# Kernel optimization log

Measured on AMD Instinct MI355X. Metric: run time of the kernel, lower is better.

## Reference

```python
import jax, jax.numpy as jnp
import numpy as np

D_MODEL = 1024
D_STATE = 64
BATCH = 4
SEQ_L = 4096
LN_EPS = 1e-5


def setup_inputs() -> dict:
    key = jax.random.key(0)
    ks = jax.random.split(key, 8)
    u = jax.random.normal(ks[0], (BATCH, SEQ_L, D_MODEL), jnp.float32)
    # Parameters mirroring StateSpaceLayer._initialize_parameters
    A_log = jax.random.uniform(ks[1], (D_STATE,), jnp.float32, -2.0, -0.1)
    xav = float(np.sqrt(6.0 / (D_STATE + D_MODEL)))
    B = jax.random.uniform(ks[2], (D_STATE, D_MODEL), jnp.float32, -xav, xav) * 0.1
    C = jax.random.uniform(ks[3], (D_MODEL, D_STATE), jnp.float32, -xav, xav) * 0.1
    D = jnp.zeros((D_MODEL,), jnp.float32)
    delta = jax.random.uniform(ks[4], (D_MODEL,), jnp.float32, 0.001, 0.1)
    gamma = jnp.ones((D_MODEL,), jnp.float32)
    beta = jnp.zeros((D_MODEL,), jnp.float32)
    freq_align = jax.random.normal(ks[5], (D_MODEL,), jnp.float32)
    reward = jax.random.normal(ks[6], (D_MODEL,), jnp.float32)
    return dict(u=u, A_log=A_log, B=B, C=C, D=D, delta=delta,
                gamma=gamma, beta=beta, freq_align=freq_align, reward=reward)


def reference(u, A_log, B, C, D, delta, gamma, beta, freq_align, reward):
    b, L, d = u.shape
    A = -jnp.exp(A_log)                                   # [N]
    # --- convolution kernel: K[k] = C @ (A_bar[0])^k, A_bar[0] = exp(delta[0]*A) ---
    k_idx = jnp.arange(L, dtype=u.dtype)                  # [L]
    powers = jnp.exp(k_idx[:, None] * (delta[0] * A)[None, :])  # [L, N]
    K = jnp.einsum('ln,dn->ld', powers, C)                # [L, D]
    # --- FFT-based causal (circular, zero-padded) convolution ---
    fft_size = 1 << int(np.ceil(np.log2(2 * L)))
    u_fft = jnp.fft.fft(u, n=fft_size, axis=1)            # [B, F, D] complex
    K_fft = jnp.fft.fft(K, n=fft_size, axis=0)            # [F, D] complex
    y = jnp.fft.ifft(u_fft * K_fft[None], axis=1).real[:, :L, :]
    # --- D skip connection ---
    y = y + u * D
    # --- FFT-based learning signals: scale spectrum, add real 'reward' to every bin ---
    y_fft = jnp.fft.fft(y, axis=1)
    y = jnp.fft.ifft(y_fft * freq_align + reward, axis=1).real
    # --- LayerNorm (eval-mode dropout = identity) ---
    mean = y.mean(-1, keepdims=True)
    var = y.var(-1, keepdims=True)
    y = (y - mean) / jnp.sqrt(var + LN_EPS) * gamma + beta
    # --- final state update with mean timescale ---
    delta_mean = delta.mean()
    A_bar_s = jnp.exp(delta_mean * A)                     # [N]
    A_safe = A + 1e-8 * jnp.sign(A)
    B_bar = ((A_bar_s - 1.0) / A_safe)[:, None] * B       # [N, D]
    state = jnp.zeros((b, A.shape[0]), u.dtype)
    final_state = A_bar_s * state + jnp.einsum('nd,bd->bn', B_bar, u[:, -1, :])
    return (y, final_state)
```

## Files before the change

### kernel.cpp

```cpp
#include <hip/hip_runtime.h>
#include <math.h>

#define BATCH  4
#define SEQL   4096
#define DMODEL 1024
#define NSTATE 64
#define LN_EPS 1e-5f
#define NCH    16
#define TCH    256
#define TB     16
#define TSUB   8

typedef unsigned short u16;
typedef unsigned int   u32;
typedef float f32x2 __attribute__((ext_vector_type(2)));

__device__ __forceinline__ f32x2 fma2(f32x2 a, f32x2 b, f32x2 c) {
#if __has_builtin(__builtin_elementwise_fma)
    return __builtin_elementwise_fma(a, b, c);
#else
    f32x2 d; d.x = fmaf(a.x, b.x, c.x); d.y = fmaf(a.y, b.y, c.y); return d;
#endif
}

__device__ __forceinline__ u16 f2bf(float x) {
    u32 b = __float_as_uint(x);
    b += 0x7FFF + ((b >> 16) & 1);
    return (u16)(b >> 16);
}
__device__ __forceinline__ float bf2f(u16 h) {
    return __uint_as_float(((u32)h) << 16);
}
__device__ __forceinline__ f32x2 unpack2bf(u32 p) {
    f32x2 v; v.x = bf2f((u16)p); v.y = bf2f((u16)(p >> 16)); return v;
}

template <bool ZBF16>
__global__ __launch_bounds__(256) void k_scan(const float* __restrict__ u,
                                              const float* __restrict__ A_log,
                                              const float* __restrict__ C,
                                              const float* __restrict__ Dvec,
                                              const float* __restrict__ delta,
                                              const float* __restrict__ fal,
                                              const float* __restrict__ rw,
                                              const float* __restrict__ Bm,
                                              u16* __restrict__ f,
                                              void* __restrict__ zout,
                                              float* __restrict__ st,
                                              int nb) {
    if (blockIdx.x >= nb) {
        const int sb = blockIdx.x - nb;
        const int n = sb & 63;
        const int b = sb >> 6;
        const int tid = threadIdx.x;
        const float* ul = u + ((size_t)b * SEQL + (SEQL - 1)) * DMODEL;
        const float* Bn = Bm + (size_t)n * DMODEL;
        float dot = 0.f, dsum = 0.f;
        for (int dd = tid; dd < DMODEL; dd += 256) {
            dot = fmaf(Bn[dd], ul[dd], dot);
            dsum += delta[dd];
        }
#pragma unroll
        for (int off = 32; off > 0; off >>= 1) {
            dot  += __shfl_down(dot,  off, 64);
            dsum += __shfl_down(dsum, off, 64);
        }
        __shared__ float red[8];
        const int wave = tid >> 6, lane = tid & 63;
        if (lane == 0) { red[wave] = dot; red[4 + wave] = dsum; }
        __syncthreads();
        if (tid == 0) {
            dot  = red[0] + red[1] + red[2] + red[3];
            dsum = red[4] + red[5] + red[6] + red[7];
            const float dmean = dsum * (1.f / DMODEL);
            const float A = -expf(A_log[n]);
            const float Abar = expf(dmean * A);
            const float Asafe = A + (A >= 0.f ? 1e-8f : -1e-8f);
            st[sb] = ((Abar - 1.f) / Asafe) * dot;
        }
        return;
    }
    __shared__ float r_lds[NSTATE];
    __shared__ float part[2][4][TB][64];
    const int tid = threadIdx.x;
    const int w = tid >> 6, l = tid & 63;
    const int b   = blockIdx.x / (16 * NCH);
    const int rem = blockIdx.x % (16 * NCH);
    const int dt  = rem / NCH;
    const int j   = rem % NCH;
    const int n0  = w << 4;
    const int d   = (dt << 6) | l;

    if (tid < NSTATE) r_lds[tid] = expf(delta[0] * -expf(A_log[tid]));
    __syncthreads();

    const float fad = fal[d];
    f32x2 r2[8], c2[8], s2[8];
#pragma unroll
    for (int p = 0; p < 8; ++p) {
        r2[p] = *(const f32x2*)&r_lds[n0 + 2 * p];
        s2[p] = (f32x2)(0.f, 0.f);
    }
#pragma unroll
    for (int p = 0; p < 8; ++p) {
        c2[p].x = fad * C[(size_t)d * NSTATE + n0 + 2*p];
        c2[p].y = fad * C[(size_t)d * NSTATE + n0 + 2*p + 1];
    }

    const float Ddf = Dvec[d] * fad;
    const float rwd = rw[d];
    const float* ub = u + ((size_t)b * SEQL + (size_t)j * TCH) * DMODEL + d;
    const size_t zoff = ((size_t)b * SEQL + (size_t)j * TCH) * DMODEL + d;
    u16*   zb16 = (u16*)zout + zoff;
    float* zb32 = (float*)zout + zoff;

    for (int tb = 0; tb < TCH / TB; ++tb) {
        const int pb = tb & 1;
        float ur[TB];
        f32x2 zr2[TB];
#pragma unroll
        for (int t = 0; t < TB; ++t) {
            ur[t] = ub[(size_t)(tb * TB + t) * DMODEL];
            zr2[t] = (f32x2)(0.f, 0.f);
        }
#pragma unroll
        for (int q = 0; q < 4; ++q) {
            f32x2 sa = s2[2*q], sb2 = s2[2*q+1];
            const f32x2 ra = r2[2*q], rb = r2[2*q+1];
            const f32x2 ca = c2[2*q], cb = c2[2*q+1];
#pragma unroll
            for (int t = 0; t < TB; ++t) {
                f32x2 u2; u2.x = ur[t]; u2.y = ur[t];
                sa  = fma2(ra, sa,  u2);
                sb2 = fma2(rb, sb2, u2);
                zr2[t] = fma2(ca, sa,  zr2[t]);
                zr2[t] = fma2(cb, sb2, zr2[t]);
            }
            s2[2*q] = sa; s2[2*q+1] = sb2;
        }
#pragma unroll
        for (int t = 0; t < TB; ++t) {
            float v = zr2[t].x + zr2[t].y;
            if (w == 0) v = fmaf(Ddf, ur[t], v);
            part[pb][w][t][l] = v;
        }
        __syncthreads();
#pragma unroll
        for (int k = 0; k < 4; ++k) {
            const int t = (w << 2) | k;
            float v = (part[pb][0][t][l] + part[pb][1][t][l]) +
                      (part[pb][2][t][l] + part[pb][3][t][l]);
            if (j == 0 && tb == 0 && t == 0) v += rwd;
            if (ZBF16) zb16[(size_t)(tb * TB + t) * DMODEL] = f2bf(v);
            else       zb32[(size_t)(tb * TB + t) * DMODEL] = v;
        }
    }
    u16* fb = f + (((size_t)b * NCH + j) * NSTATE + n0) * DMODEL + d;
#pragma unroll
    for (int p = 0; p < 8; ++p) {
        fb[(size_t)(2*p)     * DMODEL] = f2bf(s2[p].x);
        fb[(size_t)(2*p + 1) * DMODEL] = f2bf(s2[p].y);
    }
}

__global__ __launch_bounds__(256) void k_pass2w(const float* __restrict__ A_log,
                                                const float* __restrict__ delta,
                                                const float* __restrict__ C,
                                                const float* __restrict__ fal,
                                                u16* __restrict__ f) {
    const int tid = blockIdx.x * 256 + threadIdx.x;
    const int d = tid & (DMODEL - 1);
    const int n = (tid >> 10) & (NSTATE - 1);
    const int b = tid >> 16;
    const float A  = -expf(A_log[n]);
    const float rT = expf((float)TCH * delta[0] * A);
    const float fc = fal[d] * C[(size_t)d * NSTATE + n];
    float I = 0.f;
    u16* p = f + ((size_t)b * NCH * NSTATE + n) * DMODEL + d;
    const size_t stride = (size_t)NSTATE * DMODEL;
    for (int j = 0; j < NCH; ++j) {
        float tmp = bf2f(p[(size_t)j * stride]);
        p[(size_t)j * stride] = f2bf(fc * I);
        I = fmaf(rT, I, tmp);
    }
}

template <bool ZBF16>
__global__ __launch_bounds__(256) void k_corr_ln(const void* __restrict__ zin,
                                                 const u16* __restrict__ W,
                                                 const float* __restrict__ A_log,
                                                 const float* __restrict__ delta,
                                                 const float* __restrict__ gamma,
                                                 const float* __restrict__ beta,
                                                 float* __restrict__ y) {
    const int lb  = (blockIdx.x & 7) * 256 + (blockIdx.x >> 3);
    const int b   = lb >> 9;
    const int row = lb & 511;
    const int tbase = row * TSUB;
    const int j     = tbase >> 8;
    const int tloc0 = tbase & (TCH - 1);

    __shared__ float r_lds[NSTATE];
    __shared__ float pst_lds[NSTATE];
    __shared__ float red[4 * TSUB * 2];

    const int tid = threadIdx.x;
    if (tid < NSTATE) {
        const float A = -expf(A_log[tid]);
        const float d0v = delta[0];
        r_lds[tid]   = expf(d0v * A);
        pst_lds[tid] = expf((float)(tloc0 + 1) * d0v * A);
    }
    __syncthreads();

    const int d0 = tid << 2;
    f32x2 acc01[TSUB], acc23[TSUB];
#pragma unroll
    for (int t = 0; t < TSUB; ++t) {
        acc01[t] = (f32x2)(0.f, 0.f);
        acc23[t] = (f32x2)(0.f, 0.f);
    }

    if (j > 0) {
        const u16* Wb = W + (((size_t)b * NCH + j) * NSTATE) * DMODEL + d0;
#pragma unroll 2
        for (int n = 0; n < NSTATE; ++n) {
            const uint2 wv = *(const uint2*)(Wb + (size_t)n * DMODEL);
            const f32x2 w01 = unpack2bf(wv.x);
            const f32x2 w23 = unpack2bf(wv.y);
            float p = pst_lds[n];
            const float r = r_lds[n];
#pragma unroll
            for (int t = 0; t < TSUB; ++t) {
                f32x2 pp; pp.x = p; pp.y = p;
                acc01[t] = fma2(pp, w01, acc01[t]);
                acc23[t] = fma2(pp, w23, acc23[t]);
                p *= r;
            }
        }
    }

    const size_t rowoff = ((size_t)b * SEQL + tbase) * DMODEL + d0;
    float sums[TSUB], sqs[TSUB];
#pragma unroll
    for (int t = 0; t < TSUB; ++t) {
        float z0, z1, z2, z3;
        if (ZBF16) {
            const uint2 zv = *(const uint2*)((const u16*)zin + rowoff + (size_t)t * DMODEL);
            const f32x2 a = unpack2bf(zv.x), bb2 = unpack2bf(zv.y);
            z0 = a.x; z1 = a.y; z2 = bb2.x; z3 = bb2.y;
        } else {
            const float4 zv = *(const float4*)((const float*)zin + rowoff + (size_t)t * DMODEL);
            z0 = zv.x; z1 = zv.y; z2 = zv.z; z3 = zv.w;
        }
        z0 += acc01[t].x; z1 += acc01[t].y; z2 += acc23[t].x; z3 += acc23[t].y;
        acc01[t].x = z0; acc01[t].y = z1; acc23[t].x = z2; acc23[t].y = z3;
        sums[t] = (z0 + z1) + (z2 + z3);
        sqs[t]  = (z0*z0 + z1*z1) + (z2*z2 + z3*z3);
    }
    const int wave = tid >> 6, lane = tid & 63;
#pragma unroll
    for (int t = 0; t < TSUB; ++t) {
        float s = sums[t], q = sqs[t];
#pragma unroll
        for (int off = 32; off > 0; off >>= 1) {
            s += __shfl_down(s, off, 64);
            q += __shfl_down(q, off, 64);
        }
        if (lane == 0) {
            red[(wave * TSUB + t) * 2]     = s;
            red[(wave * TSUB + t) * 2 + 1] = q;
        }
    }
    __syncthreads();
    const float4 g  = *(const float4*)&gamma[d0];
    const float4 bb = *(const float4*)&beta[d0];
#pragma unroll
    for (int t = 0; t < TSUB; ++t) {
        float s = red[t * 2]     + red[(TSUB + t) * 2] +
                  red[(2 * TSUB + t) * 2] + red[(3 * TSUB + t) * 2];
        float q = red[t * 2 + 1] + red[(TSUB + t) * 2 + 1] +
                  red[(2 * TSUB + t) * 2 + 1] + red[(3 * TSUB + t) * 2 + 1];
        const float mean = s * (1.f / DMODEL);
        const float var  = q * (1.f / DMODEL) - mean * mean;
        const float inv  = 1.f / sqrtf(var + LN_EPS);
        float4 o;
        o.x = (acc01[t].x - mean) * inv * g.x + bb.x;
        o.y = (acc01[t].y - mean) * inv * g.y + bb.y;
        o.z = (acc23[t].x - mean) * inv * g.z + bb.z;
        o.w = (acc23[t].y - mean) * inv * g.w + bb.w;
        *(float4*)&y[rowoff + (size_t)t * DMODEL] = o;
    }
}

extern "C" void kernel_launch(void* const* d_in, const int* in_sizes, int n_in,
                              void* d_out, int out_size, void* d_ws, size_t ws_size,
                              hipStream_t stream) {
    const float* u     = (const float*)d_in[0];
    const float* A_log = (const float*)d_in[1];
    const float* B     = (const float*)d_in[2];
    const float* C     = (const float*)d_in[3];
    const float* Dv    = (const float*)d_in[4];
    const float* delta = (const float*)d_in[5];
    const float* gamma = (const float*)d_in[6];
    const float* beta  = (const float*)d_in[7];
    const float* fal   = (const float*)d_in[8];
    const float* rw    = (const float*)d_in[9];

    float* y  = (float*)d_out;
    float* st = y + (size_t)BATCH * SEQL * DMODEL;
    u16* f    = (u16*)d_ws;

    const int nb = BATCH * 16 * NCH;

    const size_t f_bytes = (size_t)BATCH * NCH * NSTATE * DMODEL * sizeof(u16);
    const size_t z_bytes = (size_t)BATCH * SEQL * DMODEL * sizeof(u16);
    const bool zbf16 = (f_bytes + z_bytes) <= ws_size;
    void* zbuf = zbf16 ? (void*)((char*)d_ws + f_bytes) : (void*)y;

    if (zbf16) {
        hipLaunchKernelGGL((k_scan<true>), dim3(nb + BATCH * NSTATE), dim3(256), 0, stream,
                           u, A_log, C, Dv, delta, fal, rw, B, f, zbuf, st, nb);
    } else {
        hipLaunchKernelGGL((k_scan<false>), dim3(nb + BATCH * NSTATE), dim3(256), 0, stream,
                           u, A_log, C, Dv, delta, fal, rw, B, f, zbuf, st, nb);
    }
    hipLaunchKernelGGL(k_pass2w, dim3(BATCH * NSTATE * DMODEL / 256), dim3(256), 0, stream,
                       A_log, delta, C, fal, f);
    if (zbf16) {
        hipLaunchKernelGGL((k_corr_ln<true>), dim3(BATCH * (SEQL / TSUB)), dim3(256), 0, stream,
                           zbuf, f, A_log, delta, gamma, beta, y);
    } else {
        hipLaunchKernelGGL((k_corr_ln<false>), dim3(BATCH * (SEQL / TSUB)), dim3(256), 0, stream,
                           zbuf, f, A_log, delta, gamma, beta, y);
    }
}
```

Before: 115.2 us.

## Compute chunk correction with bf16 MFMA and transpose carry-state layout

```diff
diff --git a/kernel.cpp b/kernel.cpp
--- a/kernel.cpp
+++ b/kernel.cpp
@@ -9,11 +9,14 @@
 #define NCH    16
 #define TCH    256
 #define TB     16
-#define TSUB   8
+#define TSUB   16
+#define PPAD   80
 
 typedef unsigned short u16;
 typedef unsigned int   u32;
 typedef float f32x2 __attribute__((ext_vector_type(2)));
+typedef float f32x4 __attribute__((ext_vector_type(4)));
+typedef short bf16x8 __attribute__((ext_vector_type(8)));
 
 __device__ __forceinline__ f32x2 fma2(f32x2 a, f32x2 b, f32x2 c) {
 #if __has_builtin(__builtin_elementwise_fma)
@@ -31,8 +34,8 @@
 __device__ __forceinline__ float bf2f(u16 h) {
     return __uint_as_float(((u32)h) << 16);
 }
-__device__ __forceinline__ f32x2 unpack2bf(u32 p) {
-    f32x2 v; v.x = bf2f((u16)p); v.y = bf2f((u16)(p >> 16)); return v;
+__device__ __forceinline__ u32 pack2bf(f32x2 v) {
+    return (u32)f2bf(v.x) | ((u32)f2bf(v.y) << 16);
 }
 
 template <bool ZBF16>
@@ -155,11 +158,13 @@
             else       zb32[(size_t)(tb * TB + t) * DMODEL] = v;
         }
     }
-    u16* fb = f + (((size_t)b * NCH + j) * NSTATE + n0) * DMODEL + d;
-#pragma unroll
-    for (int p = 0; p < 8; ++p) {
-        fb[(size_t)(2*p)     * DMODEL] = f2bf(s2[p].x);
-        fb[(size_t)(2*p + 1) * DMODEL] = f2bf(s2[p].y);
+    {
+        u32 packed[8];
+#pragma unroll
+        for (int p = 0; p < 8; ++p) packed[p] = pack2bf(s2[p]);
+        u16* fb = f + (((size_t)b * NCH + j) * DMODEL + d) * NSTATE + n0;
+        *(uint4*)(fb)     = *(uint4*)&packed[0];
+        *(uint4*)(fb + 8) = *(uint4*)&packed[4];
     }
 }
 
@@ -168,16 +173,16 @@
                                                 const float* __restrict__ C,
                                                 const float* __restrict__ fal,
                                                 u16* __restrict__ f) {
-    const int tid = blockIdx.x * 256 + threadIdx.x;
-    const int d = tid & (DMODEL - 1);
-    const int n = (tid >> 10) & (NSTATE - 1);
-    const int b = tid >> 16;
+    const int g = blockIdx.x * 256 + threadIdx.x;
+    const int n = g & (NSTATE - 1);
+    const int d = (g >> 6) & (DMODEL - 1);
+    const int b = g >> 16;
     const float A  = -expf(A_log[n]);
     const float rT = expf((float)TCH * delta[0] * A);
     const float fc = fal[d] * C[(size_t)d * NSTATE + n];
     float I = 0.f;
-    u16* p = f + ((size_t)b * NCH * NSTATE + n) * DMODEL + d;
-    const size_t stride = (size_t)NSTATE * DMODEL;
+    u16* p = f + (((size_t)b * NCH) * DMODEL + d) * NSTATE + n;
+    const size_t stride = (size_t)DMODEL * NSTATE;
     for (int j = 0; j < NCH; ++j) {
         float tmp = bf2f(p[(size_t)j * stride]);
         p[(size_t)j * stride] = f2bf(fc * I);
@@ -193,103 +198,91 @@
                                                  const float* __restrict__ gamma,
                                                  const float* __restrict__ beta,
                                                  float* __restrict__ y) {
-    const int lb  = (blockIdx.x & 7) * 256 + (blockIdx.x >> 3);
-    const int b   = lb >> 9;
-    const int row = lb & 511;
-    const int tbase = row * TSUB;
-    const int j     = tbase >> 8;
-    const int tloc0 = tbase & (TCH - 1);
-
-    __shared__ float r_lds[NSTATE];
-    __shared__ float pst_lds[NSTATE];
-    __shared__ float red[4 * TSUB * 2];
+    __shared__ float relay[TSUB][DMODEL];
+    __shared__ u16   p_lds[TSUB * PPAD];
+    __shared__ float red[4][TSUB][2];
 
     const int tid = threadIdx.x;
-    if (tid < NSTATE) {
-        const float A = -expf(A_log[tid]);
-        const float d0v = delta[0];
-        r_lds[tid]   = expf(d0v * A);
-        pst_lds[tid] = expf((float)(tloc0 + 1) * d0v * A);
+    const int w = tid >> 6, l = tid & 63;
+    const int x = blockIdx.x & 7;
+    const int m = blockIdx.x >> 3;
+    const int s = x + ((m >> 4) << 3);
+    const int b = s >> 4;
+    const int j = s & (NCH - 1);
+    const int unit = m & 15;
+    const int tbase = j * TCH + unit * TSUB;
+    const int tloc0 = unit * TSUB;
+
+    const float d0v = delta[0];
+    for (int i = tid; i < TSUB * NSTATE; i += 256) {
+        const int t = i >> 6, n = i & 63;
+        const float A = -expf(A_log[n]);
+        p_lds[t * PPAD + n] = f2bf(expf((float)(tloc0 + t + 1) * d0v * A));
     }
     __syncthreads();
 
-    const int d0 = tid << 2;
-    f32x2 acc01[TSUB], acc23[TSUB];
-#pragma unroll
-    for (int t = 0; t < TSUB; ++t) {
-        acc01[t] = (f32x2)(0.f, 0.f);
-        acc23[t] = (f32x2)(0.f, 0.f);
-    }
-
-    if (j > 0) {
-        const u16* Wb = W + (((size_t)b * NCH + j) * NSTATE) * DMODEL + d0;
-#pragma unroll 2
-        for (int n = 0; n < NSTATE; ++n) {
-            const uint2 wv = *(const uint2*)(Wb + (size_t)n * DMODEL);
-            const f32x2 w01 = unpack2bf(wv.x);
-            const f32x2 w23 = unpack2bf(wv.y);
-            float p = pst_lds[n];
-            const float r = r_lds[n];
-#pragma unroll
-            for (int t = 0; t < TSUB; ++t) {
-                f32x2 pp; pp.x = p; pp.y = p;
-                acc01[t] = fma2(pp, w01, acc01[t]);
-                acc23[t] = fma2(pp, w23, acc23[t]);
-                p *= r;
-            }
-        }
-    }
-
-    const size_t rowoff = ((size_t)b * SEQL + tbase) * DMODEL + d0;
-    float sums[TSUB], sqs[TSUB];
-#pragma unroll
-    for (int t = 0; t < TSUB; ++t) {
-        float z0, z1, z2, z3;
-        if (ZBF16) {
-            const uint2 zv = *(const uint2*)((const u16*)zin + rowoff + (size_t)t * DMODEL);
-            const f32x2 a = unpack2bf(zv.x), bb2 = unpack2bf(zv.y);
-            z0 = a.x; z1 = a.y; z2 = bb2.x; z3 = bb2.y;
-        } else {
-            const float4 zv = *(const float4*)((const float*)zin + rowoff + (size_t)t * DMODEL);
-            z0 = zv.x; z1 = zv.y; z2 = zv.z; z3 = zv.w;
-        }
-        z0 += acc01[t].x; z1 += acc01[t].y; z2 += acc23[t].x; z3 += acc23[t].y;
-        acc01[t].x = z0; acc01[t].y = z1; acc23[t].x = z2; acc23[t].y = z3;
-        sums[t] = (z0 + z1) + (z2 + z3);
-        sqs[t]  = (z0*z0 + z1*z1) + (z2*z2 + z3*z3);
-    }
-    const int wave = tid >> 6, lane = tid & 63;
-#pragma unroll
-    for (int t = 0; t < TSUB; ++t) {
-        float s = sums[t], q = sqs[t];
-#pragma unroll
-        for (int off = 32; off > 0; off >>= 1) {
-            s += __shfl_down(s, off, 64);
-            q += __shfl_down(q, off, 64);
-        }
-        if (lane == 0) {
-            red[(wave * TSUB + t) * 2]     = s;
-            red[(wave * TSUB + t) * 2 + 1] = q;
+    const int colsub = l & 15, rgrp = l >> 4;
+    bf16x8 a0 = *(const bf16x8*)(p_lds + (l & 15) * PPAD + ((l >> 4) << 3));
+    bf16x8 a1 = *(const bf16x8*)(p_lds + (l & 15) * PPAD + 32 + ((l >> 4) << 3));
+
+    float rs[4] = {0.f, 0.f, 0.f, 0.f}, rq[4] = {0.f, 0.f, 0.f, 0.f};
+
+#pragma unroll 1
+    for (int dt = 0; dt < 16; ++dt) {
+        const int dcol = (w << 8) + (dt << 4) + colsub;
+        f32x4 acc = {0.f, 0.f, 0.f, 0.f};
+        if (j > 0) {
+            const u16* wt = W + (((size_t)b * NCH + j) * DMODEL + dcol) * NSTATE;
+            const bf16x8 b0 = *(const bf16x8*)(wt + ((l >> 4) << 3));
+            const bf16x8 b1 = *(const bf16x8*)(wt + 32 + ((l >> 4) << 3));
+            acc = __builtin_amdgcn_mfma_f32_16x16x32_bf16(a0, b0, acc, 0, 0, 0);
+            acc = __builtin_amdgcn_mfma_f32_16x16x32_bf16(a1, b1, acc, 0, 0, 0);
+        }
+#pragma unroll
+        for (int reg = 0; reg < 4; ++reg) {
+            const int trow = (rgrp << 2) + reg;
+            const size_t zi = ((size_t)b * SEQL + tbase + trow) * DMODEL + dcol;
+            float v = acc[reg];
+            v += ZBF16 ? bf2f(((const u16*)zin)[zi]) : ((const float*)zin)[zi];
+            relay[trow][dcol] = v;
+            rs[reg] += v;
+            rq[reg] += v * v;
+        }
+    }
+#pragma unroll
+    for (int reg = 0; reg < 4; ++reg) {
+        float s2 = rs[reg], q2 = rq[reg];
+#pragma unroll
+        for (int off = 1; off < 16; off <<= 1) {
+            s2 += __shfl_xor(s2, off, 64);
+            q2 += __shfl_xor(q2, off, 64);
+        }
+        if (colsub == 0) {
+            red[w][(rgrp << 2) + reg][0] = s2;
+            red[w][(rgrp << 2) + reg][1] = q2;
         }
     }
     __syncthreads();
-    const float4 g  = *(const float4*)&gamma[d0];
-    const float4 bb = *(const float4*)&beta[d0];
-#pragma unroll
-    for (int t = 0; t < TSUB; ++t) {
-        float s = red[t * 2]     + red[(TSUB + t) * 2] +
-                  red[(2 * TSUB + t) * 2] + red[(3 * TSUB + t) * 2];
-        float q = red[t * 2 + 1] + red[(TSUB + t) * 2 + 1] +
-                  red[(2 * TSUB + t) * 2 + 1] + red[(3 * TSUB + t) * 2 + 1];
-        const float mean = s * (1.f / DMODEL);
-        const float var  = q * (1.f / DMODEL) - mean * mean;
+
+    const int d4 = tid << 2;
+    const float4 g4  = *(const float4*)&gamma[d4];
+    const float4 bb4 = *(const float4*)&beta[d4];
+#pragma unroll 1
+    for (int trow = 0; trow < TSUB; ++trow) {
+        const float sv = (red[0][trow][0] + red[1][trow][0]) +
+                         (red[2][trow][0] + red[3][trow][0]);
+        const float qv = (red[0][trow][1] + red[1][trow][1]) +
+                         (red[2][trow][1] + red[3][trow][1]);
+        const float mean = sv * (1.f / DMODEL);
+        const float var  = qv * (1.f / DMODEL) - mean * mean;
         const float inv  = 1.f / sqrtf(var + LN_EPS);
+        const float4 vv = *(const float4*)&relay[trow][d4];
         float4 o;
-        o.x = (acc01[t].x - mean) * inv * g.x + bb.x;
-        o.y = (acc01[t].y - mean) * inv * g.y + bb.y;
-        o.z = (acc23[t].x - mean) * inv * g.z + bb.z;
-        o.w = (acc23[t].y - mean) * inv * g.w + bb.w;
-        *(float4*)&y[rowoff + (size_t)t * DMODEL] = o;
+        o.x = (vv.x - mean) * inv * g4.x + bb4.x;
+        o.y = (vv.y - mean) * inv * g4.y + bb4.y;
+        o.z = (vv.z - mean) * inv * g4.z + bb4.z;
+        o.w = (vv.w - mean) * inv * g4.w + bb4.w;
+        *(float4*)&y[((size_t)b * SEQL + tbase + trow) * DMODEL + d4] = o;
     }
 }
 
```

New measurement: 119.8 us. 4.0% more time.
